# Kernel optimization log

Measured on AMD Instinct MI355X. Metric: run time of the kernel, lower is better.

Reference implementation:

```python
import jax, jax.numpy as jnp
import numpy as np

THRESH = 1.0
GAMA = 1.0
TAU0 = 0.5

# ZIF surrogate spike: forward hard step, backward triangular surrogate
@jax.custom_vjp
def zif(x):
    return (x > 0).astype(x.dtype)

def _zif_fwd(x):
    return zif(x), x

def _zif_bwd(x, g):
    surr = (1.0 / GAMA) * (1.0 / GAMA) * jnp.clip(GAMA - jnp.abs(x), 0.0, None)
    return (g * surr,)

zif.defvjp(_zif_fwd, _zif_bwd)


def setup_inputs() -> dict:
    key = jax.random.key(0)
    k1, k2, k3, k4, k5 = jax.random.split(key, 5)
    B, T, C, H, W = 32, 8, 128, 32, 32
    red = 4
    x = jax.random.normal(k1, (B, T, C, H, W), dtype=jnp.float32)
    # fc1: Linear(C, C//red); fc2: Linear(C//red, 1); PyTorch default init scale
    s1 = 1.0 / np.sqrt(C)
    s2 = 1.0 / np.sqrt(C // red)
    w1 = jax.random.uniform(k2, (C // red, C), jnp.float32, -s1, s1)
    b1 = jax.random.uniform(k3, (C // red,), jnp.float32, -s1, s1)
    w2 = jax.random.uniform(k4, (1, C // red), jnp.float32, -s2, s2)
    b2 = jax.random.uniform(k5, (1,), jnp.float32, -s2, s2)
    return {"x": x, "w1": w1, "b1": b1, "w2": w2, "b2": b2}


def reference(x, w1, b1, w2, b2):
    B, T, C, H, W = x.shape

    def step(carry, xt):
        mem, tau = carry  # mem: [B,C,H,W], tau: [B,1,1,1]
        mem = mem * tau + xt
        # SE-style gating MLP on channel means
        x_mean = jnp.mean(mem, axis=(-1, -2))          # [B,C]
        embed = jax.nn.relu(x_mean @ w1.T + b1)        # [B,C//r]
        lifp = jax.nn.sigmoid(embed @ w2.T + b2)       # [B,1]
        new_tau = lifp[:, :, None, None]               # [B,1,1,1]
        spike = zif(mem - THRESH)
        mem = (1.0 - spike) * mem
        return (mem, new_tau), spike

    mem0 = jnp.zeros((B, C, H, W), dtype=x.dtype)
    tau0 = jnp.full((B, 1, 1, 1), TAU0, dtype=x.dtype)
    xt = jnp.transpose(x, (1, 0, 2, 3, 4))  # [T,B,C,H,W]
    _, spikes = jax.lax.scan(step, (mem0, tau0), xt)
    return jnp.transpose(spikes, (1, 0, 2, 3, 4))  # [B,T,C,H,W]
```

## Files before the change

kernel.cpp:

```cpp
#include <hip/hip_runtime.h>

typedef float v4f __attribute__((ext_vector_type(4)));

#define NB   32
#define NT   8
#define NC   128
#define NQ   256
#define CRED 32
#define PADI 32

#define NWORDS (2 * NB * NC * 2)

__device__ int                g_arrive[NB * PADI];
__device__ unsigned long long g_xw[NWORDS];

__global__ __launch_bounds__(256)
void lif_init() {
    int i = threadIdx.x + blockIdx.x * blockDim.x;
    if (i < NWORDS) g_xw[i] = 0ull;
    if (i < NB * PADI) g_arrive[i] = 0;
}

__global__ __launch_bounds__(256, 4)
void dynamic_lif(const float* __restrict__ x,
                 const float* __restrict__ w1,
                 const float* __restrict__ b1,
                 const float* __restrict__ w2,
                 const float* __restrict__ b2,
                 float* __restrict__ out)
{
    const int bid = blockIdx.x;
    const int b   = bid >> 5;
    const int c0  = (bid & 31) << 2;
    const int tid = threadIdx.x;
    const int wv  = tid >> 6;
    const int ln  = tid & 63;

    __shared__ double       s_part[4][4];
    __shared__ unsigned int s_w[256];
    __shared__ double       s_xm[NC];
    __shared__ float        s_tau;

    const v4f* __restrict__ x4 = (const v4f*)x;
    v4f* __restrict__ o4       = (v4f*)out;

    v4f mem[4];
    #pragma unroll
    for (int p = 0; p < 4; ++p) mem[p] = (v4f){0.f, 0.f, 0.f, 0.f};

    float tau = 0.5f;

    v4f xv[4];
    #pragma unroll
    for (int p = 0; p < 4; ++p)
        xv[p] = __builtin_nontemporal_load(x4 + ((b * NT + 0) * NC + c0 + p) * NQ + tid);

    for (int t = 0; t < NT; ++t) {
        double psum[4];
        #pragma unroll
        for (int p = 0; p < 4; ++p) {
            v4f m = mem[p];
            m.x = fmaf(m.x, tau, xv[p].x);
            m.y = fmaf(m.y, tau, xv[p].y);
            m.z = fmaf(m.z, tau, xv[p].z);
            m.w = fmaf(m.w, tau, xv[p].w);
            psum[p] = ((double)m.x + (double)m.y) + ((double)m.z + (double)m.w);
            v4f sp;
            sp.x = (m.x > 1.0f) ? 1.0f : 0.0f;
            sp.y = (m.y > 1.0f) ? 1.0f : 0.0f;
            sp.z = (m.z > 1.0f) ? 1.0f : 0.0f;
            sp.w = (m.w > 1.0f) ? 1.0f : 0.0f;
            __builtin_nontemporal_store(sp, o4 + ((b * NT + t) * NC + c0 + p) * NQ + tid);
            m.x = (m.x > 1.0f) ? 0.0f : m.x;
            m.y = (m.y > 1.0f) ? 0.0f : m.y;
            m.z = (m.z > 1.0f) ? 0.0f : m.z;
            m.w = (m.w > 1.0f) ? 0.0f : m.w;
            mem[p] = m;
        }

        if (t + 1 < NT) {
            #pragma unroll
            for (int p = 0; p < 4; ++p)
                xv[p] = __builtin_nontemporal_load(
                    x4 + ((b * NT + (t + 1)) * NC + c0 + p) * NQ + tid);
        }

        #pragma unroll
        for (int p = 0; p < 4; ++p) {
            double s = psum[p];
            #pragma unroll
            for (int off = 32; off > 0; off >>= 1) s += __shfl_down(s, off);
            if (ln == 0) s_part[p][wv] = s;
        }
        __syncthreads();
        if (tid < 4) {
            double s = (s_part[tid][0] + s_part[tid][1]) +
                       (s_part[tid][2] + s_part[tid][3]);
            double mean = s * (1.0 / 1024.0);
            unsigned long long bits = __double_as_longlong(mean);
            unsigned long long tag  = ((unsigned long long)(t + 1)) << 32;
            const int base = (((t & 1) * (NB * NC)) + b * NC + c0 + tid) * 2;
            __hip_atomic_store(&g_xw[base + 0], tag | (bits & 0xffffffffull),
                               __ATOMIC_RELAXED, __HIP_MEMORY_SCOPE_AGENT);
            __hip_atomic_store(&g_xw[base + 1], tag | (bits >> 32),
                               __ATOMIC_RELAXED, __HIP_MEMORY_SCOPE_AGENT);
        }
        __syncthreads();

        if (t == NT - 1) break;

        if (tid == 0) {
            __hip_atomic_fetch_add(&g_arrive[b * PADI], 1,
                                   __ATOMIC_RELAXED, __HIP_MEMORY_SCOPE_AGENT);
            const int target = 32 * (t + 1);
            while (__hip_atomic_load(&g_arrive[b * PADI],
                                     __ATOMIC_RELAXED, __HIP_MEMORY_SCOPE_AGENT) < target)
                __builtin_amdgcn_s_sleep(2);
        }
        __syncthreads();

        {
            const int idx = (((t & 1) * (NB * NC)) + b * NC + (tid >> 1)) * 2
                            + (tid & 1);
            const unsigned int want = (unsigned int)(t + 1);
            unsigned long long w;
            for (;;) {
                w = __hip_atomic_load(&g_xw[idx], __ATOMIC_RELAXED,
                                      __HIP_MEMORY_SCOPE_AGENT);
                if ((unsigned int)(w >> 32) == want) break;
                __builtin_amdgcn_s_sleep(1);
            }
            s_w[tid] = (unsigned int)w;
        }
        __syncthreads();
        if (tid < NC) {
            unsigned long long bits =
                ((unsigned long long)s_w[2 * tid + 1] << 32) | s_w[2 * tid];
            s_xm[tid] = __longlong_as_double(bits);
        }
        __syncthreads();

        double e = 0.0;
        if (tid < CRED) {
            const v4f* __restrict__ w1v = (const v4f*)(w1 + tid * NC);
            double acc = (double)b1[tid];
            #pragma unroll
            for (int q = 0; q < NC / 4; ++q) {
                v4f wq = w1v[q];
                acc += s_xm[4 * q + 0] * (double)wq.x;
                acc += s_xm[4 * q + 1] * (double)wq.y;
                acc += s_xm[4 * q + 2] * (double)wq.z;
                acc += s_xm[4 * q + 3] * (double)wq.w;
            }
            double emb = acc > 0.0 ? acc : 0.0;
            e = emb * (double)w2[tid];
        }
        #pragma unroll
        for (int off = 32; off > 0; off >>= 1) e += __shfl_down(e, off);
        if (tid == 0) {
            double z = e + (double)b2[0];
            s_tau = (float)(1.0 / (1.0 + exp(-z)));
        }
        __syncthreads();
        tau = s_tau;
    }
}

extern "C" void kernel_launch(void* const* d_in, const int* in_sizes, int n_in,
                              void* d_out, int out_size, void* d_ws, size_t ws_size,
                              hipStream_t stream) {
    const float* x  = (const float*)d_in[0];
    const float* w1 = (const float*)d_in[1];
    const float* b1 = (const float*)d_in[2];
    const float* w2 = (const float*)d_in[3];
    const float* b2 = (const float*)d_in[4];
    float* out      = (float*)d_out;

    hipLaunchKernelGGL(lif_init, dim3((NWORDS + 255) / 256), dim3(256),
                       0, stream);
    hipLaunchKernelGGL(dynamic_lif, dim3(NB * NC / 4), dim3(256), 0, stream,
                       x, w1, b1, w2, b2, out);
}
```

Baseline: 284.7 us.

## Drop per-batch arrival counter, index mean slots per timestep, trim barriers

Removes the global arrival counter and its spin-wait. Each timestep now writes to its own slot in a per-t buffer, and the tagged-word poll on that slot is the only cross-block synchronization. The s_xm staging pass and several __syncthreads are dropped: the doubles are rebuilt inline from s_w, and LDS-only barriers built from s_waitcnt lgkmcnt(0) plus s_barrier replace the remaining ones. The aim is to shorten the per-step grid synchronization latency, at the cost of a larger global buffer and reliance on the hand-written barrier's memory semantics.

```diff
diff --git a/kernel.cpp b/kernel.cpp
--- a/kernel.cpp
+++ b/kernel.cpp
@@ -7,19 +7,18 @@
 #define NC   128
 #define NQ   256
 #define CRED 32
-#define PADI 32
 
-#define NWORDS (2 * NB * NC * 2)
+#define NWORDS (NT * NB * NC * 2)
 
-__device__ int                g_arrive[NB * PADI];
 __device__ unsigned long long g_xw[NWORDS];
 
 __global__ __launch_bounds__(256)
 void lif_init() {
     int i = threadIdx.x + blockIdx.x * blockDim.x;
     if (i < NWORDS) g_xw[i] = 0ull;
-    if (i < NB * PADI) g_arrive[i] = 0;
 }
+
+#define LDS_BARRIER() asm volatile("s_waitcnt lgkmcnt(0)\n\ts_barrier" ::: "memory")
 
 __global__ __launch_bounds__(256, 4)
 void dynamic_lif(const float* __restrict__ x,
@@ -38,7 +37,6 @@
 
     __shared__ double       s_part[4][4];
     __shared__ unsigned int s_w[256];
-    __shared__ double       s_xm[NC];
     __shared__ float        s_tau;
 
     const v4f* __restrict__ x4 = (const v4f*)x;
@@ -92,53 +90,36 @@
             for (int off = 32; off > 0; off >>= 1) s += __shfl_down(s, off);
             if (ln == 0) s_part[p][wv] = s;
         }
-        __syncthreads();
+        LDS_BARRIER();
+
+        if (t == NT - 1) break;
+
         if (tid < 4) {
             double s = (s_part[tid][0] + s_part[tid][1]) +
                        (s_part[tid][2] + s_part[tid][3]);
             double mean = s * (1.0 / 1024.0);
             unsigned long long bits = __double_as_longlong(mean);
             unsigned long long tag  = ((unsigned long long)(t + 1)) << 32;
-            const int base = (((t & 1) * (NB * NC)) + b * NC + c0 + tid) * 2;
+            const int base = ((t * NB + b) * NC + c0 + tid) * 2;
             __hip_atomic_store(&g_xw[base + 0], tag | (bits & 0xffffffffull),
                                __ATOMIC_RELAXED, __HIP_MEMORY_SCOPE_AGENT);
             __hip_atomic_store(&g_xw[base + 1], tag | (bits >> 32),
                                __ATOMIC_RELAXED, __HIP_MEMORY_SCOPE_AGENT);
         }
-        __syncthreads();
-
-        if (t == NT - 1) break;
-
-        if (tid == 0) {
-            __hip_atomic_fetch_add(&g_arrive[b * PADI], 1,
-                                   __ATOMIC_RELAXED, __HIP_MEMORY_SCOPE_AGENT);
-            const int target = 32 * (t + 1);
-            while (__hip_atomic_load(&g_arrive[b * PADI],
-                                     __ATOMIC_RELAXED, __HIP_MEMORY_SCOPE_AGENT) < target)
-                __builtin_amdgcn_s_sleep(2);
-        }
-        __syncthreads();
 
         {
-            const int idx = (((t & 1) * (NB * NC)) + b * NC + (tid >> 1)) * 2
-                            + (tid & 1);
+            const int idx = ((t * NB + b) * NC + (tid >> 1)) * 2 + (tid & 1);
             const unsigned int want = (unsigned int)(t + 1);
             unsigned long long w;
             for (;;) {
                 w = __hip_atomic_load(&g_xw[idx], __ATOMIC_RELAXED,
                                       __HIP_MEMORY_SCOPE_AGENT);
                 if ((unsigned int)(w >> 32) == want) break;
-                __builtin_amdgcn_s_sleep(1);
+                __builtin_amdgcn_s_sleep(2);
             }
             s_w[tid] = (unsigned int)w;
         }
-        __syncthreads();
-        if (tid < NC) {
-            unsigned long long bits =
-                ((unsigned long long)s_w[2 * tid + 1] << 32) | s_w[2 * tid];
-            s_xm[tid] = __longlong_as_double(bits);
-        }
-        __syncthreads();
+        LDS_BARRIER();
 
         double e = 0.0;
         if (tid < CRED) {
@@ -147,10 +128,15 @@
             #pragma unroll
             for (int q = 0; q < NC / 4; ++q) {
                 v4f wq = w1v[q];
-                acc += s_xm[4 * q + 0] * (double)wq.x;
-                acc += s_xm[4 * q + 1] * (double)wq.y;
-                acc += s_xm[4 * q + 2] * (double)wq.z;
-                acc += s_xm[4 * q + 3] * (double)wq.w;
+                #pragma unroll
+                for (int k = 0; k < 4; ++k) {
+                    const int c = 4 * q + k;
+                    unsigned long long bits =
+                        ((unsigned long long)s_w[2 * c + 1] << 32) | s_w[2 * c];
+                    double xm = __longlong_as_double(bits);
+                    acc += xm * (double)((k == 0) ? wq.x : (k == 1) ? wq.y
+                                         : (k == 2) ? wq.z : wq.w);
+                }
             }
             double emb = acc > 0.0 ? acc : 0.0;
             e = emb * (double)w2[tid];
@@ -161,7 +147,7 @@
             double z = e + (double)b2[0];
             s_tau = (float)(1.0 / (1.0 + exp(-z)));
         }
-        __syncthreads();
+        LDS_BARRIER();
         tau = s_tau;
     }
 }
```

Result: faster. 276.9 us (-2.7%).
